# Optimization experiments

Measured on AMD Instinct MI355X. Metric: run time of the kernel, lower is better.

## Reference

```python
import jax, jax.numpy as jnp
import numpy as np

B, S, T, V, E, H = 32, 64, 64, 32000, 256, 512


def lstm_layer(x, h0, c0, Wih, Whh, bih, bhh):
    """PyTorch-convention LSTM layer. x: [B,T,in]; gates order i,f,g,o."""
    xg = jnp.einsum('bti,gi->btg', x, Wih) + (bih + bhh)  # [B,T,4H] precomputed input gates

    def step(carry, xt):
        h, c = carry
        g = xt + h @ Whh.T
        i, f, gg, o = jnp.split(g, 4, axis=-1)
        c = jax.nn.sigmoid(f) * c + jax.nn.sigmoid(i) * jnp.tanh(gg)
        h = jax.nn.sigmoid(o) * jnp.tanh(c)
        return (h, c), h

    (hT, cT), ys = jax.lax.scan(step, (h0, c0), xg.transpose(1, 0, 2))
    return ys.transpose(1, 0, 2), hT, cT


def setup_inputs() -> dict:
    key = jax.random.key(0)
    ks = jax.random.split(key, 32)
    w = lambda k, shape: jax.random.normal(k, shape, jnp.float32) * 0.05
    return {
        'source': jax.random.randint(ks[0], (B, S), 0, V),
        'target': jax.random.randint(ks[1], (B, T), 0, V),
        'enc_emb': w(ks[2], (V, E)),
        'enc_Wih0': w(ks[3], (4 * H, E)),
        'enc_Whh0': w(ks[4], (4 * H, H)),
        'enc_bih0': w(ks[5], (4 * H,)),
        'enc_bhh0': w(ks[6], (4 * H,)),
        'enc_Wih1': w(ks[7], (4 * H, H)),
        'enc_Whh1': w(ks[8], (4 * H, H)),
        'enc_bih1': w(ks[9], (4 * H,)),
        'enc_bhh1': w(ks[10], (4 * H,)),
        'dec_emb': w(ks[11], (V, E)),
        'dec_Wih0': w(ks[12], (4 * H, E)),
        'dec_Whh0': w(ks[13], (4 * H, H)),
        'dec_bih0': w(ks[14], (4 * H,)),
        'dec_bhh0': w(ks[15], (4 * H,)),
        'dec_Wih1': w(ks[16], (4 * H, H)),
        'dec_Whh1': w(ks[17], (4 * H, H)),
        'dec_bih1': w(ks[18], (4 * H,)),
        'dec_bhh1': w(ks[19], (4 * H,)),
        'aff_W': w(ks[20], (V, H)),
        'aff_b': w(ks[21], (V,)),
    }


def reference(source, target, enc_emb, enc_Wih0, enc_Whh0, enc_bih0, enc_bhh0,
              enc_Wih1, enc_Whh1, enc_bih1, enc_bhh1, dec_emb,
              dec_Wih0, dec_Whh0, dec_bih0, dec_bhh0,
              dec_Wih1, dec_Whh1, dec_bih1, dec_bhh1, aff_W, aff_b):
    b = source.shape[0]
    z = jnp.zeros((b, H), jnp.float32)
    # Encoder: 2-layer LSTM over source, keep final (h,c) per layer
    x = enc_emb[source]                                   # [B,S,E]
    y0, h0, c0 = lstm_layer(x, z, z, enc_Wih0, enc_Whh0, enc_bih0, enc_bhh0)
    _, h1, c1 = lstm_layer(y0, z, z, enc_Wih1, enc_Whh1, enc_bih1, enc_bhh1)
    # Decoder: original loop is always teacher-forced (input = target[:, i]),
    # so it equals one full-sequence LSTM over target[:, :-1].
    dx = dec_emb[target[:, :-1]]                          # [B,T-1,E]
    d0, _, _ = lstm_layer(dx, h0, c0, dec_Wih0, dec_Whh0, dec_bih0, dec_bhh0)
    d1, _, _ = lstm_layer(d0, h1, c1, dec_Wih1, dec_Whh1, dec_bih1, dec_bhh1)
    logits = jnp.einsum('bth,vh->btv', d1, aff_W) + aff_b  # [B,T-1,V]
    # outputs[:,0,:] stays zero as in the original
    return jnp.concatenate([jnp.zeros((b, 1, logits.shape[-1]), logits.dtype), logits], axis=1)
```

## Files before the change

kernel.cpp:

```cpp
#include <hip/hip_runtime.h>
#include <hip/hip_bf16.h>

using bf16 = __hip_bfloat16;
typedef __bf16 bf16x8 __attribute__((ext_vector_type(8)));
typedef float f32x4 __attribute__((ext_vector_type(4)));
typedef int i32x4 __attribute__((ext_vector_type(4)));
typedef short short4v __attribute__((ext_vector_type(4)));
typedef short short8v __attribute__((ext_vector_type(8)));

#define DEV __device__ __forceinline__


DEV unsigned short f2bf(float f) {
  unsigned u = __builtin_bit_cast(unsigned, f);
  u = (u + 0x7fffu + ((u >> 16) & 1u)) >> 16;
  return (unsigned short)u;
}

DEV f32x4 mfma16(bf16x8 a, bf16x8 b, f32x4 c) {
  return __builtin_amdgcn_mfma_f32_16x16x32_bf16(a, b, c, 0, 0, 0);
}

DEV void llc_load16(bf16x8* dst, const bf16* p) {
  i32x4 r;
  asm volatile("global_load_dwordx4 %0, %1, off sc0 sc1" : "=v"(r) : "v"(p) : "memory");
  *dst = __builtin_bit_cast(bf16x8, r);
}
DEV void g_load16(bf16x8* dst, const bf16* p) {
  i32x4 r;
  asm volatile("global_load_dwordx4 %0, %1, off" : "=v"(r) : "v"(p) : "memory");
  *dst = __builtin_bit_cast(bf16x8, r);
}
DEV void llc_store16(void* p, short8v v) {
  asm volatile("global_store_dwordx4 %0, %1, off sc0 sc1"
               :: "v"(p), "v"(__builtin_bit_cast(i32x4, v)) : "memory");
}
DEV void llc_store_f32(float* p, float v) {
  asm volatile("global_store_dword %0, %1, off sc0 sc1" :: "v"(p), "v"(v) : "memory");
}
DEV bool valid16(bf16x8 v) {
  i32x4 u = __builtin_bit_cast(i32x4, v);
  return (u[0] != -1) && (u[1] != -1) && (u[2] != -1) && (u[3] != -1);
}

DEV void poll_slab(const bf16* base, int fl, int koff, bf16x8 a0[4], bf16x8 a1[4]) {
  const bf16* r0 = base + (long)fl * 512 + koff;
  const bf16* r1 = base + (long)(fl + 16) * 512 + koff;
#pragma unroll
  for (int kt = 0; kt < 4; ++kt) {
    llc_load16(&a0[kt], r0 + kt * 32);
    llc_load16(&a1[kt], r1 + kt * 32);
  }
  asm volatile("s_waitcnt vmcnt(0)" ::: "memory");
  {
    bool ok = true;
#pragma unroll
    for (int kt = 0; kt < 4; ++kt) ok = ok && valid16(a0[kt]) && valid16(a1[kt]);
    if (__all(ok)) return;
  }
  while (true) {
    unsigned s0, s1, s2, s3;
    asm volatile(
        "global_load_dword %0, %4, off sc0 sc1\n\t"
        "global_load_dword %1, %5, off sc0 sc1\n\t"
        "global_load_dword %2, %6, off sc0 sc1\n\t"
        "global_load_dword %3, %7, off sc0 sc1\n\t"
        "s_waitcnt vmcnt(0)"
        : "=v"(s0), "=v"(s1), "=v"(s2), "=v"(s3)
        : "v"(r0), "v"(r0 + 32), "v"(r0 + 64), "v"(r0 + 96)
        : "memory");
    bool ok = (s0 != 0xFFFFFFFFu) & (s1 != 0xFFFFFFFFu) & (s2 != 0xFFFFFFFFu) &
              (s3 != 0xFFFFFFFFu);
    if (__all(ok)) break;
    __builtin_amdgcn_s_sleep(1);
  }
  while (true) {
#pragma unroll
    for (int kt = 0; kt < 4; ++kt) {
      llc_load16(&a0[kt], r0 + kt * 32);
      llc_load16(&a1[kt], r1 + kt * 32);
    }
    asm volatile("s_waitcnt vmcnt(0)" ::: "memory");
    bool ok = true;
#pragma unroll
    for (int kt = 0; kt < 4; ++kt) ok = ok && valid16(a0[kt]) && valid16(a1[kt]);
    if (__all(ok)) break;
    __builtin_amdgcn_s_sleep(1);
  }
}
DEV float llc_poll_f32(const float* p) {
  while (true) {
    float r;
    asm volatile("global_load_dword %0, %1, off sc0 sc1\n\ts_waitcnt vmcnt(0)"
                 : "=v"(r) : "v"(p) : "memory");
    if (__all(__builtin_bit_cast(unsigned, r) != 0xFFFFFFFFu)) return r;
    __builtin_amdgcn_s_sleep(1);
  }
}

DEV bf16* swz(bf16* base, int row, int colbyte) {
  return (bf16*)((char*)base + row * 128 + (colbyte ^ ((row & 7) << 4)));
}

struct ConvJobs {
  const float* src[9];
  bf16* dst[9];
  int n[9];
  int cnt;
};

__global__ void convert_all(ConvJobs jobs) {
  long base = (long)blockIdx.x * blockDim.x + threadIdx.x;
  long stride = (long)gridDim.x * blockDim.x;
  for (int ji = 0; ji < jobs.cnt; ++ji) {
    const float* s = jobs.src[ji];
    bf16* d = jobs.dst[ji];
    long n4 = (long)jobs.n[ji] >> 2;
    for (long i = base; i < n4; i += stride) {
      f32x4 v = *(const f32x4*)(s + i * 4);
      short4v o;
#pragma unroll
      for (int j = 0; j < 4; ++j) o[j] = (short)f2bf(v[j]);
      *(short4v*)((short*)d + i * 4) = o;
    }
  }
}

__global__ void embed_gather(const int* __restrict__ ids, const float* __restrict__ emb,
                             bf16* __restrict__ out, int rows, int ids_stride) {
  long total = (long)rows * 64;
  long stride = (long)gridDim.x * blockDim.x;
  for (long i = (long)blockIdx.x * blockDim.x + threadIdx.x; i < total; i += stride) {
    int row = (int)(i >> 6);
    int e = ((int)i & 63) * 4;
    int b = row & 31;
    int t = row >> 5;
    int id = ids[b * ids_stride + t];
    f32x4 v = *(const f32x4*)(emb + (long)id * 256 + e);
    short4v o;
#pragma unroll
    for (int j = 0; j < 4; ++j) o[j] = (short)f2bf(v[j]);
    *(short4v*)((short*)out + (long)row * 256 + e) = o;
  }
}

__global__ void zero_t0(float* __restrict__ out) {
  long total = 32l * 8000;
  long stride = (long)gridDim.x * blockDim.x;
  f32x4 z{};
  for (long i = (long)blockIdx.x * blockDim.x + threadIdx.x; i < total; i += stride) {
    long b = i / 8000;
    long v = i - b * 8000;
    *(f32x4*)(out + b * 64 * 32000 + v * 4) = z;
  }
}

__launch_bounds__(256)
__global__ void gemm_aff(const bf16* __restrict__ Ag, const bf16* __restrict__ Wg,
                         const float* __restrict__ affb, float* __restrict__ out) {
  __shared__ __align__(16) bf16 As[128 * 64];
  __shared__ __align__(16) bf16 Bs[128 * 64];
  int mt = blockIdx.x & 15;
  int ns = blockIdx.x >> 4;
  long m0 = (long)mt * 128, gn0 = (long)ns * 128;
  int tid = threadIdx.x;
  int lane = tid & 63, wave = tid >> 6;
  int wm = wave & 1, wn = wave >> 1;
  int fl = lane & 15, fg = lane >> 4;

  if (mt == 0) {
    f32x4 z{};
#pragma unroll
    for (int idx = 0; idx < 4; ++idx) {
      int i = idx * 256 + tid;
      int r = i >> 5, c4 = i & 31;
      *(f32x4*)(out + (long)r * 64 * 32000 + gn0 + c4 * 4) = z;
    }
  }

  f32x4 acc[4][4] = {};
  bf16x8 areg[4], wreg[4];
  int rowv[4], colv[4];
#pragma unroll
  for (int i = 0; i < 4; ++i) {
    int e = (i * 256 + tid) * 8;
    rowv[i] = e >> 6; colv[i] = e & 63;
    long ar = m0 + rowv[i]; if (ar >= 2016) ar = 2015;
    g_load16(&areg[i], Ag + ar * 512 + colv[i]);
    g_load16(&wreg[i], Wg + (gn0 + rowv[i]) * 512 + colv[i]);
  }
  for (int k0 = 0; k0 < 512; k0 += 64) {
    asm volatile("s_waitcnt vmcnt(0)" ::: "memory");
    __syncthreads();
#pragma unroll
    for (int i = 0; i < 4; ++i) {
      *(bf16x8*)swz(As, rowv[i], colv[i] * 2) = areg[i];
      *(bf16x8*)swz(Bs, rowv[i], colv[i] * 2) = wreg[i];
    }
    __syncthreads();
    if (k0 + 64 < 512) {
#pragma unroll
      for (int i = 0; i < 4; ++i) {
        long ar = m0 + rowv[i]; if (ar >= 2016) ar = 2015;
        g_load16(&areg[i], Ag + ar * 512 + (k0 + 64) + colv[i]);
        g_load16(&wreg[i], Wg + (gn0 + rowv[i]) * 512 + (k0 + 64) + colv[i]);
      }
    }
#pragma unroll
    for (int kt = 0; kt < 2; ++kt) {
      bf16x8 af[4], bfr[4];
#pragma unroll
      for (int x = 0; x < 4; ++x)
        af[x] = *(const bf16x8*)swz(As, wm * 64 + x * 16 + fl, (kt * 32 + fg * 8) * 2);
#pragma unroll
      for (int x = 0; x < 4; ++x)
        bfr[x] = *(const bf16x8*)swz(Bs, wn * 64 + x * 16 + fl, (kt * 32 + fg * 8) * 2);
#pragma unroll
      for (int mi = 0; mi < 4; ++mi)
#pragma unroll
        for (int ni = 0; ni < 4; ++ni)
          acc[mi][ni] = mfma16(af[mi], bfr[ni], acc[mi][ni]);
    }
  }
#pragma unroll
  for (int mi = 0; mi < 4; ++mi)
#pragma unroll
    for (int ni = 0; ni < 4; ++ni)
#pragma unroll
      for (int r = 0; r < 4; ++r) {
        long row = m0 + wm * 64 + mi * 16 + fg * 4 + r;
        long col = gn0 + wn * 64 + ni * 16 + fl;
        if (row < 2016) {
          float v = acc[mi][ni][r] + affb[col];
          long orow = (long)(row & 31) * 64 + (row >> 5) + 1;
          out[orow * 32000 + col] = v;
        }
      }
}

__launch_bounds__(256)
__global__ void gemm_fb(const bf16* __restrict__ A, const float* __restrict__ Wf,
                        const float* __restrict__ bias1, float* __restrict__ C,
                        int M, int N, int K) {
  __shared__ __align__(16) bf16 As[128][64];
  __shared__ __align__(16) bf16 Bs[128][64];
  int nm = (M + 127) >> 7;
  int mt_blk = blockIdx.x % nm;
  int nt_blk = blockIdx.x / nm;
  long m0 = (long)mt_blk * 128, n0 = (long)nt_blk * 128;
  int tid = threadIdx.x;
  int lane = tid & 63, wave = tid >> 6;
  int wm = wave & 1, wn = wave >> 1;
  int fl = lane & 15, fg = lane >> 4;
  f32x4 acc[4][4] = {};
  for (int k0 = 0; k0 < K; k0 += 64) {
    __syncthreads();
#pragma unroll
    for (int i = 0; i < 4; ++i) {
      int e = (i * 256 + tid) * 8;
      int row = e >> 6, col = e & 63;
      long ar = m0 + row; if (ar >= M) ar = M - 1;
      *(bf16x8*)(&As[row][col]) = *(const bf16x8*)(A + ar * (long)K + k0 + col);
      long br = n0 + row; if (br >= N) br = N - 1;
      const float* p = Wf + br * (long)K + k0 + col;
      f32x4 v0 = *(const f32x4*)p, v1 = *(const f32x4*)(p + 4);
      short8v o;
#pragma unroll
      for (int j = 0; j < 4; ++j) { o[j] = (short)f2bf(v0[j]); o[j + 4] = (short)f2bf(v1[j]); }
      *(short8v*)(&Bs[row][col]) = o;
    }
    __syncthreads();
#pragma unroll
    for (int kt = 0; kt < 2; ++kt) {
      bf16x8 af[4], bfr[4];
#pragma unroll
      for (int x = 0; x < 4; ++x)
        af[x] = *(const bf16x8*)(&As[wm * 64 + x * 16 + fl][kt * 32 + fg * 8]);
#pragma unroll
      for (int x = 0; x < 4; ++x)
        bfr[x] = *(const bf16x8*)(&Bs[wn * 64 + x * 16 + fl][kt * 32 + fg * 8]);
#pragma unroll
      for (int mi = 0; mi < 4; ++mi)
#pragma unroll
        for (int ni = 0; ni < 4; ++ni)
          acc[mi][ni] = mfma16(af[mi], bfr[ni], acc[mi][ni]);
    }
  }
#pragma unroll
  for (int mi = 0; mi < 4; ++mi)
#pragma unroll
    for (int ni = 0; ni < 4; ++ni)
#pragma unroll
      for (int r = 0; r < 4; ++r) {
        long row = m0 + wm * 64 + mi * 16 + fg * 4 + r;
        long col = n0 + wn * 64 + ni * 16 + fl;
        if (row < M && col < N) {
          float v = acc[mi][ni][r] + bias1[col];
          long orow = (long)(row & 31) * 64 + (row >> 5) + 1;
          C[orow * (long)N + col] = v;
        }
      }
}

struct FusedParams {
  const bf16* wih[4]; const bf16* whh[4];
  const float* bih[4]; const float* bhh[4];
  const bf16* x[4];
  bf16* y[4];
  const bf16* hinit[4];
  const float* cinit[4];
  float* cfin[4];
};

__launch_bounds__(256)
__global__ void lstm_fused(FusedParams P) {
  __shared__ float part[4][32][33];
  __shared__ __align__(16) unsigned short h_sh[32][8];
  const int tid = threadIdx.x;
  const int lane = tid & 63, wave = tid >> 6;
  const int fl = lane & 15, fg = lane >> 4;
  const int l = blockIdx.x >> 6;
  const int slc = blockIdx.x & 63;
  const int n0 = slc * 8;
  const int b_t = tid & 31, d_t = tid >> 5;
  const int T = (l < 2) ? 64 : 63;
  const int Kx = (l & 1) ? 512 : 256;
  const int xspan = Kx >> 2;
  const int ktx = xspan >> 5;
  const bf16* __restrict__ Wih = P.wih[l];
  const bf16* __restrict__ Whh = P.whh[l];
  const bf16* __restrict__ X = P.x[l];
  bf16* __restrict__ Y = P.y[l];
  const bf16* __restrict__ Hinit = P.hinit[l];

  float bsum[4];
#pragma unroll
  for (int gi = 0; gi < 4; ++gi)
    bsum[gi] = P.bih[l][gi * 512 + n0 + d_t] + P.bhh[l][gi * 512 + n0 + d_t];

  bf16x8 wfx[2][4], wfh[2][4];
#pragma unroll
  for (int nt = 0; nt < 2; ++nt) {
    int j = nt * 16 + fl;
    long row = (long)(j >> 3) * 512 + n0 + (j & 7);
#pragma unroll
    for (int kt = 0; kt < 4; ++kt) {
      if (kt < ktx)
        wfx[nt][kt] =
            *(const bf16x8*)(Wih + row * (long)Kx + wave * xspan + kt * 32 + fg * 8);
      wfh[nt][kt] = *(const bf16x8*)(Whh + row * 512l + wave * 128 + kt * 32 + fg * 8);
    }
  }
  float c = 0.f;

  for (int t = 0; t < T; ++t) {
    const bf16* xb = X + (long)t * 32 * Kx;
    f32x4 acc[2][2] = {};
    if (l & 1) {
      bf16x8 xa0[4], xa1[4];
      poll_slab(xb, fl, wave * 128 + fg * 8, xa0, xa1);
#pragma unroll
      for (int kt = 0; kt < 4; ++kt) {
        acc[0][0] = mfma16(xa0[kt], wfx[0][kt], acc[0][0]);
        acc[0][1] = mfma16(xa0[kt], wfx[1][kt], acc[0][1]);
        acc[1][0] = mfma16(xa1[kt], wfx[0][kt], acc[1][0]);
        acc[1][1] = mfma16(xa1[kt], wfx[1][kt], acc[1][1]);
      }
    } else {
      bf16x8 xa0[2], xa1[2];
#pragma unroll
      for (int kt = 0; kt < 2; ++kt) {
        int k = wave * xspan + kt * 32 + fg * 8;
        xa0[kt] = *(const bf16x8*)(xb + (long)fl * Kx + k);
        xa1[kt] = *(const bf16x8*)(xb + (long)(fl + 16) * Kx + k);
      }
#pragma unroll
      for (int kt = 0; kt < 2; ++kt) {
        acc[0][0] = mfma16(xa0[kt], wfx[0][kt], acc[0][0]);
        acc[0][1] = mfma16(xa0[kt], wfx[1][kt], acc[0][1]);
        acc[1][0] = mfma16(xa1[kt], wfx[0][kt], acc[1][0]);
        acc[1][1] = mfma16(xa1[kt], wfx[1][kt], acc[1][1]);
      }
    }

    const bf16* hb = (t == 0) ? Hinit : (Y + (long)(t - 1) * 32 * 512);
    bf16x8 ha0[4], ha1[4];
    poll_slab(hb, fl, wave * 128 + fg * 8, ha0, ha1);
    if (t == 0) c = llc_poll_f32(P.cinit[l] + (long)b_t * 512 + n0 + d_t);
#pragma unroll
    for (int kt = 0; kt < 4; ++kt) {
      acc[0][0] = mfma16(ha0[kt], wfh[0][kt], acc[0][0]);
      acc[0][1] = mfma16(ha0[kt], wfh[1][kt], acc[0][1]);
      acc[1][0] = mfma16(ha1[kt], wfh[0][kt], acc[1][0]);
      acc[1][1] = mfma16(ha1[kt], wfh[1][kt], acc[1][1]);
    }
#pragma unroll
    for (int mt = 0; mt < 2; ++mt)
#pragma unroll
      for (int nt = 0; nt < 2; ++nt)
#pragma unroll
        for (int r = 0; r < 4; ++r)
          part[wave][mt * 16 + fg * 4 + r][nt * 16 + fl] = acc[mt][nt][r];
    __syncthreads();

    float g4[4];
#pragma unroll
    for (int gi = 0; gi < 4; ++gi) {
      int j = gi * 8 + d_t;
      g4[gi] = part[0][b_t][j] + part[1][b_t][j] + part[2][b_t][j] + part[3][b_t][j] +
               bsum[gi];
    }
    float ig = 1.f / (1.f + __expf(-g4[0]));
    float ff = 1.f / (1.f + __expf(-g4[1]));
    float gg = tanhf(g4[2]);
    float og = 1.f / (1.f + __expf(-g4[3]));
    c = ff * c + ig * gg;
    float h = og * tanhf(c);
    h_sh[b_t][d_t] = f2bf(h);
    if (t == T - 1)
      llc_store_f32(P.cfin[l] + (long)b_t * 512 + n0 + d_t, c);
    __syncthreads();
    if (wave == 0 && lane < 32)
      llc_store16((unsigned short*)Y + ((long)t * 32 + lane) * 512 + n0,
                  *(const short8v*)(&h_sh[lane][0]));
  }
}

extern "C" void kernel_launch(void* const* d_in, const int* in_sizes, int n_in,
                              void* d_out, int out_size, void* d_ws, size_t ws_size,
                              hipStream_t stream) {
  (void)in_sizes; (void)n_in; (void)out_size;
  const int*   source   = (const int*)d_in[0];
  const int*   target   = (const int*)d_in[1];
  const float* enc_emb  = (const float*)d_in[2];
  const float* enc_Wih0 = (const float*)d_in[3];
  const float* enc_Whh0 = (const float*)d_in[4];
  const float* enc_bih0 = (const float*)d_in[5];
  const float* enc_bhh0 = (const float*)d_in[6];
  const float* enc_Wih1 = (const float*)d_in[7];
  const float* enc_Whh1 = (const float*)d_in[8];
  const float* enc_bih1 = (const float*)d_in[9];
  const float* enc_bhh1 = (const float*)d_in[10];
  const float* dec_emb  = (const float*)d_in[11];
  const float* dec_Wih0 = (const float*)d_in[12];
  const float* dec_Whh0 = (const float*)d_in[13];
  const float* dec_bih0 = (const float*)d_in[14];
  const float* dec_bhh0 = (const float*)d_in[15];
  const float* dec_Wih1 = (const float*)d_in[16];
  const float* dec_Whh1 = (const float*)d_in[17];
  const float* dec_bih1 = (const float*)d_in[18];
  const float* dec_bhh1 = (const float*)d_in[19];
  const float* aff_W    = (const float*)d_in[20];
  const float* aff_b    = (const float*)d_in[21];
  float* out = (float*)d_out;

  size_t off = 0;
  auto alc = [&](size_t bytes) {
    char* p = (char*)d_ws + off;
    off += (bytes + 255) & ~(size_t)255;
    return (void*)p;
  };
  bf16*  ZH  = (bf16*)alc(32 * 512 * 2);
  float* ZC  = (float*)alc(32 * 512 * 4);
  size_t zero_span = off;
  size_t poison_begin = off;
  float* CE0 = (float*)alc(32 * 512 * 4);
  float* CE1 = (float*)alc(32 * 512 * 4);
  bf16*  YE0 = (bf16*)alc((size_t)2048 * 512 * 2);
  bf16*  YE1 = (bf16*)alc((size_t)2048 * 512 * 2);
  bf16*  YD0 = (bf16*)alc((size_t)2016 * 512 * 2);
  bf16*  YD1 = (bf16*)alc((size_t)2016 * 512 * 2);
  size_t poison_end = off;
  float* CD  = (float*)alc(32 * 512 * 4);
  float* CD2 = (float*)alc(32 * 512 * 4);
  bf16*  XE  = (bf16*)alc((size_t)2048 * 256 * 2);
  bf16*  XD  = (bf16*)alc((size_t)2016 * 256 * 2);
  bf16*  WI0E = (bf16*)alc((size_t)2048 * 256 * 2);
  bf16*  WH0E = (bf16*)alc((size_t)2048 * 512 * 2);
  bf16*  WI1E = (bf16*)alc((size_t)2048 * 512 * 2);
  bf16*  WH1E = (bf16*)alc((size_t)2048 * 512 * 2);
  bf16*  WI0D = (bf16*)alc((size_t)2048 * 256 * 2);
  bf16*  WH0D = (bf16*)alc((size_t)2048 * 512 * 2);
  bf16*  WI1D = (bf16*)alc((size_t)2048 * 512 * 2);
  bf16*  WH1D = (bf16*)alc((size_t)2048 * 512 * 2);
  bf16*  WAFF = (bf16*)alc((size_t)32000 * 512 * 2);
  bool use_waff = (off <= ws_size);

  hipMemsetAsync(d_ws, 0, zero_span, stream);
  hipMemsetAsync((char*)d_ws + poison_begin, 0xFF, poison_end - poison_begin, stream);

  ConvJobs cj;
  cj.src[0] = enc_Wih0; cj.dst[0] = WI0E; cj.n[0] = 2048 * 256;
  cj.src[1] = enc_Whh0; cj.dst[1] = WH0E; cj.n[1] = 2048 * 512;
  cj.src[2] = enc_Wih1; cj.dst[2] = WI1E; cj.n[2] = 2048 * 512;
  cj.src[3] = enc_Whh1; cj.dst[3] = WH1E; cj.n[3] = 2048 * 512;
  cj.src[4] = dec_Wih0; cj.dst[4] = WI0D; cj.n[4] = 2048 * 256;
  cj.src[5] = dec_Whh0; cj.dst[5] = WH0D; cj.n[5] = 2048 * 512;
  cj.src[6] = dec_Wih1; cj.dst[6] = WI1D; cj.n[6] = 2048 * 512;
  cj.src[7] = dec_Whh1; cj.dst[7] = WH1D; cj.n[7] = 2048 * 512;
  cj.cnt = 8;
  if (use_waff) {
    cj.src[8] = aff_W; cj.dst[8] = WAFF; cj.n[8] = 32000 * 512; cj.cnt = 9;
  }
  convert_all<<<dim3(1024), dim3(256), 0, stream>>>(cj);

  embed_gather<<<dim3(512), dim3(256), 0, stream>>>(source, enc_emb, XE, 2048, 64);
  embed_gather<<<dim3(512), dim3(256), 0, stream>>>(target, dec_emb, XD, 2016, 64);
  if (!use_waff) zero_t0<<<dim3(1000), dim3(256), 0, stream>>>(out);

  FusedParams P;
  P.wih[0] = WI0E; P.whh[0] = WH0E; P.bih[0] = enc_bih0; P.bhh[0] = enc_bhh0;
  P.wih[1] = WI1E; P.whh[1] = WH1E; P.bih[1] = enc_bih1; P.bhh[1] = enc_bhh1;
  P.wih[2] = WI0D; P.whh[2] = WH0D; P.bih[2] = dec_bih0; P.bhh[2] = dec_bhh0;
  P.wih[3] = WI1D; P.whh[3] = WH1D; P.bih[3] = dec_bih1; P.bhh[3] = dec_bhh1;
  P.x[0] = XE;  P.x[1] = YE0; P.x[2] = XD;  P.x[3] = YD0;
  P.y[0] = YE0; P.y[1] = YE1; P.y[2] = YD0; P.y[3] = YD1;
  P.hinit[0] = ZH; P.hinit[1] = ZH;
  P.hinit[2] = YE0 + (size_t)63 * 32 * 512;
  P.hinit[3] = YE1 + (size_t)63 * 32 * 512;
  P.cinit[0] = ZC;  P.cinit[1] = ZC;  P.cinit[2] = CE0; P.cinit[3] = CE1;
  P.cfin[0]  = CE0; P.cfin[1]  = CE1; P.cfin[2]  = CD;  P.cfin[3]  = CD2;
  void* args[1] = {&P};
  hipLaunchCooperativeKernel((void*)lstm_fused, dim3(256), dim3(256), args, 0, stream);

  if (use_waff)
    gemm_aff<<<dim3(16 * 250), dim3(256), 0, stream>>>(YD1, WAFF, aff_b, out);
  else
    gemm_fb<<<dim3(16 * 250), dim3(256), 0, stream>>>(YD1, aff_W, aff_b, out,
                                                      2016, 32000, 512);
}
```

Before: 638.0 us.

## Fuse fp32-to-bf16 weight conversion into LSTM and projection kernels, remap GEMM tiles

Removes the separate convert_all pass and its bf16 weight buffers. The LSTM kernel now converts fp32 weights to bf16 while loading them into registers, and the output-projection GEMM converts fp32 W tiles on the fly before writing them to shared memory. The GEMM block index is remapped so groups of 8 N-tiles iterate over all 16 M-tiles, which should improve L2 reuse of the weights; the grid is padded to 4096 with early exits. The GEMM now reads twice the weight bytes and does conversion math 16 times per weight tile, trading that for skipping one full conversion kernel and its write and re-read of a 32 MB buffer.

Result: slower. 704.8 us (+10.5%).

```diff
diff --git a/kernel.cpp b/kernel.cpp
--- a/kernel.cpp
+++ b/kernel.cpp
@@ -19,6 +19,14 @@
 
 DEV f32x4 mfma16(bf16x8 a, bf16x8 b, f32x4 c) {
   return __builtin_amdgcn_mfma_f32_16x16x32_bf16(a, b, c, 0, 0, 0);
+}
+
+DEV bf16x8 cvt8(const float* p) {
+  f32x4 a = *(const f32x4*)p, b = *(const f32x4*)(p + 4);
+  short8v o;
+#pragma unroll
+  for (int j = 0; j < 4; ++j) { o[j] = (short)f2bf(a[j]); o[j + 4] = (short)f2bf(b[j]); }
+  return __builtin_bit_cast(bf16x8, o);
 }
 
 DEV void llc_load16(bf16x8* dst, const bf16* p) {
@@ -102,30 +110,6 @@
   return (bf16*)((char*)base + row * 128 + (colbyte ^ ((row & 7) << 4)));
 }
 
-struct ConvJobs {
-  const float* src[9];
-  bf16* dst[9];
-  int n[9];
-  int cnt;
-};
-
-__global__ void convert_all(ConvJobs jobs) {
-  long base = (long)blockIdx.x * blockDim.x + threadIdx.x;
-  long stride = (long)gridDim.x * blockDim.x;
-  for (int ji = 0; ji < jobs.cnt; ++ji) {
-    const float* s = jobs.src[ji];
-    bf16* d = jobs.dst[ji];
-    long n4 = (long)jobs.n[ji] >> 2;
-    for (long i = base; i < n4; i += stride) {
-      f32x4 v = *(const f32x4*)(s + i * 4);
-      short4v o;
-#pragma unroll
-      for (int j = 0; j < 4; ++j) o[j] = (short)f2bf(v[j]);
-      *(short4v*)((short*)d + i * 4) = o;
-    }
-  }
-}
-
 __global__ void embed_gather(const int* __restrict__ ids, const float* __restrict__ emb,
                              bf16* __restrict__ out, int rows, int ids_stride) {
   long total = (long)rows * 64;
@@ -144,24 +128,15 @@
   }
 }
 
-__global__ void zero_t0(float* __restrict__ out) {
-  long total = 32l * 8000;
-  long stride = (long)gridDim.x * blockDim.x;
-  f32x4 z{};
-  for (long i = (long)blockIdx.x * blockDim.x + threadIdx.x; i < total; i += stride) {
-    long b = i / 8000;
-    long v = i - b * 8000;
-    *(f32x4*)(out + b * 64 * 32000 + v * 4) = z;
-  }
-}
-
 __launch_bounds__(256)
-__global__ void gemm_aff(const bf16* __restrict__ Ag, const bf16* __restrict__ Wg,
+__global__ void gemm_aff(const bf16* __restrict__ Ag, const float* __restrict__ Wf,
                          const float* __restrict__ affb, float* __restrict__ out) {
   __shared__ __align__(16) bf16 As[128 * 64];
   __shared__ __align__(16) bf16 Bs[128 * 64];
-  int mt = blockIdx.x & 15;
-  int ns = blockIdx.x >> 4;
+  int b = blockIdx.x;
+  int ns = (b & 7) + 8 * (b >> 7);
+  int mt = (b >> 3) & 15;
+  if (ns >= 250) return;
   long m0 = (long)mt * 128, gn0 = (long)ns * 128;
   int tid = threadIdx.x;
   int lane = tid & 63, wave = tid >> 6;
@@ -179,7 +154,8 @@
   }
 
   f32x4 acc[4][4] = {};
-  bf16x8 areg[4], wreg[4];
+  bf16x8 areg[4];
+  f32x4 wv0[4], wv1[4];
   int rowv[4], colv[4];
 #pragma unroll
   for (int i = 0; i < 4; ++i) {
@@ -187,7 +163,9 @@
     rowv[i] = e >> 6; colv[i] = e & 63;
     long ar = m0 + rowv[i]; if (ar >= 2016) ar = 2015;
     g_load16(&areg[i], Ag + ar * 512 + colv[i]);
-    g_load16(&wreg[i], Wg + (gn0 + rowv[i]) * 512 + colv[i]);
+    const float* p = Wf + (gn0 + rowv[i]) * 512l + colv[i];
+    wv0[i] = *(const f32x4*)p;
+    wv1[i] = *(const f32x4*)(p + 4);
   }
   for (int k0 = 0; k0 < 512; k0 += 64) {
     asm volatile("s_waitcnt vmcnt(0)" ::: "memory");
@@ -195,7 +173,13 @@
 #pragma unroll
     for (int i = 0; i < 4; ++i) {
       *(bf16x8*)swz(As, rowv[i], colv[i] * 2) = areg[i];
-      *(bf16x8*)swz(Bs, rowv[i], colv[i] * 2) = wreg[i];
+      short8v o;
+#pragma unroll
+      for (int j = 0; j < 4; ++j) {
+        o[j] = (short)f2bf(wv0[i][j]);
+        o[j + 4] = (short)f2bf(wv1[i][j]);
+      }
+      *(short8v*)swz(Bs, rowv[i], colv[i] * 2) = o;
     }
     __syncthreads();
     if (k0 + 64 < 512) {
@@ -203,7 +187,9 @@
       for (int i = 0; i < 4; ++i) {
         long ar = m0 + rowv[i]; if (ar >= 2016) ar = 2015;
         g_load16(&areg[i], Ag + ar * 512 + (k0 + 64) + colv[i]);
-        g_load16(&wreg[i], Wg + (gn0 + rowv[i]) * 512 + (k0 + 64) + colv[i]);
+        const float* p = Wf + (gn0 + rowv[i]) * 512l + (k0 + 64) + colv[i];
+        wv0[i] = *(const f32x4*)p;
+        wv1[i] = *(const f32x4*)(p + 4);
       }
     }
 #pragma unroll
@@ -238,72 +224,8 @@
       }
 }
 
-__launch_bounds__(256)
-__global__ void gemm_fb(const bf16* __restrict__ A, const float* __restrict__ Wf,
-                        const float* __restrict__ bias1, float* __restrict__ C,
-                        int M, int N, int K) {
-  __shared__ __align__(16) bf16 As[128][64];
-  __shared__ __align__(16) bf16 Bs[128][64];
-  int nm = (M + 127) >> 7;
-  int mt_blk = blockIdx.x % nm;
-  int nt_blk = blockIdx.x / nm;
-  long m0 = (long)mt_blk * 128, n0 = (long)nt_blk * 128;
-  int tid = threadIdx.x;
-  int lane = tid & 63, wave = tid >> 6;
-  int wm = wave & 1, wn = wave >> 1;
-  int fl = lane & 15, fg = lane >> 4;
-  f32x4 acc[4][4] = {};
-  for (int k0 = 0; k0 < K; k0 += 64) {
-    __syncthreads();
-#pragma unroll
-    for (int i = 0; i < 4; ++i) {
-      int e = (i * 256 + tid) * 8;
-      int row = e >> 6, col = e & 63;
-      long ar = m0 + row; if (ar >= M) ar = M - 1;
-      *(bf16x8*)(&As[row][col]) = *(const bf16x8*)(A + ar * (long)K + k0 + col);
-      long br = n0 + row; if (br >= N) br = N - 1;
-      const float* p = Wf + br * (long)K + k0 + col;
-      f32x4 v0 = *(const f32x4*)p, v1 = *(const f32x4*)(p + 4);
-      short8v o;
-#pragma unroll
-      for (int j = 0; j < 4; ++j) { o[j] = (short)f2bf(v0[j]); o[j + 4] = (short)f2bf(v1[j]); }
-      *(short8v*)(&Bs[row][col]) = o;
-    }
-    __syncthreads();
-#pragma unroll
-    for (int kt = 0; kt < 2; ++kt) {
-      bf16x8 af[4], bfr[4];
-#pragma unroll
-      for (int x = 0; x < 4; ++x)
-        af[x] = *(const bf16x8*)(&As[wm * 64 + x * 16 + fl][kt * 32 + fg * 8]);
-#pragma unroll
-      for (int x = 0; x < 4; ++x)
-        bfr[x] = *(const bf16x8*)(&Bs[wn * 64 + x * 16 + fl][kt * 32 + fg * 8]);
-#pragma unroll
-      for (int mi = 0; mi < 4; ++mi)
-#pragma unroll
-        for (int ni = 0; ni < 4; ++ni)
-          acc[mi][ni] = mfma16(af[mi], bfr[ni], acc[mi][ni]);
-    }
-  }
-#pragma unroll
-  for (int mi = 0; mi < 4; ++mi)
-#pragma unroll
-    for (int ni = 0; ni < 4; ++ni)
-#pragma unroll
-      for (int r = 0; r < 4; ++r) {
-        long row = m0 + wm * 64 + mi * 16 + fg * 4 + r;
-        long col = n0 + wn * 64 + ni * 16 + fl;
-        if (row < M && col < N) {
-          float v = acc[mi][ni][r] + bias1[col];
-          long orow = (long)(row & 31) * 64 + (row >> 5) + 1;
-          C[orow * (long)N + col] = v;
-        }
-      }
-}
-
 struct FusedParams {
-  const bf16* wih[4]; const bf16* whh[4];
+  const float* wih[4]; const float* whh[4];
   const float* bih[4]; const float* bhh[4];
   const bf16* x[4];
   bf16* y[4];
@@ -327,8 +249,8 @@
   const int Kx = (l & 1) ? 512 : 256;
   const int xspan = Kx >> 2;
   const int ktx = xspan >> 5;
-  const bf16* __restrict__ Wih = P.wih[l];
-  const bf16* __restrict__ Whh = P.whh[l];
+  const float* __restrict__ WihF = P.wih[l];
+  const float* __restrict__ WhhF = P.whh[l];
   const bf16* __restrict__ X = P.x[l];
   bf16* __restrict__ Y = P.y[l];
   const bf16* __restrict__ Hinit = P.hinit[l];
@@ -346,9 +268,8 @@
 #pragma unroll
     for (int kt = 0; kt < 4; ++kt) {
       if (kt < ktx)
-        wfx[nt][kt] =
-            *(const bf16x8*)(Wih + row * (long)Kx + wave * xspan + kt * 32 + fg * 8);
-      wfh[nt][kt] = *(const bf16x8*)(Whh + row * 512l + wave * 128 + kt * 32 + fg * 8);
+        wfx[nt][kt] = cvt8(WihF + row * (long)Kx + wave * xspan + kt * 32 + fg * 8);
+      wfh[nt][kt] = cvt8(WhhF + row * 512l + wave * 128 + kt * 32 + fg * 8);
     }
   }
   float c = 0.f;
@@ -429,7 +350,7 @@
 extern "C" void kernel_launch(void* const* d_in, const int* in_sizes, int n_in,
                               void* d_out, int out_size, void* d_ws, size_t ws_size,
                               hipStream_t stream) {
-  (void)in_sizes; (void)n_in; (void)out_size;
+  (void)in_sizes; (void)n_in; (void)out_size; (void)ws_size;
   const int*   source   = (const int*)d_in[0];
   const int*   target   = (const int*)d_in[1];
   const float* enc_emb  = (const float*)d_in[2];
@@ -475,44 +396,18 @@
   float* CD2 = (float*)alc(32 * 512 * 4);
   bf16*  XE  = (bf16*)alc((size_t)2048 * 256 * 2);
   bf16*  XD  = (bf16*)alc((size_t)2016 * 256 * 2);
-  bf16*  WI0E = (bf16*)alc((size_t)2048 * 256 * 2);
-  bf16*  WH0E = (bf16*)alc((size_t)2048 * 512 * 2);
-  bf16*  WI1E = (bf16*)alc((size_t)2048 * 512 * 2);
-  bf16*  WH1E = (bf16*)alc((size_t)2048 * 512 * 2);
-  bf16*  WI0D = (bf16*)alc((size_t)2048 * 256 * 2);
-  bf16*  WH0D = (bf16*)alc((size_t)2048 * 512 * 2);
-  bf16*  WI1D = (bf16*)alc((size_t)2048 * 512 * 2);
-  bf16*  WH1D = (bf16*)alc((size_t)2048 * 512 * 2);
-  bf16*  WAFF = (bf16*)alc((size_t)32000 * 512 * 2);
-  bool use_waff = (off <= ws_size);
 
   hipMemsetAsync(d_ws, 0, zero_span, stream);
   hipMemsetAsync((char*)d_ws + poison_begin, 0xFF, poison_end - poison_begin, stream);
 
-  ConvJobs cj;
-  cj.src[0] = enc_Wih0; cj.dst[0] = WI0E; cj.n[0] = 2048 * 256;
-  cj.src[1] = enc_Whh0; cj.dst[1] = WH0E; cj.n[1] = 2048 * 512;
-  cj.src[2] = enc_Wih1; cj.dst[2] = WI1E; cj.n[2] = 2048 * 512;
-  cj.src[3] = enc_Whh1; cj.dst[3] = WH1E; cj.n[3] = 2048 * 512;
-  cj.src[4] = dec_Wih0; cj.dst[4] = WI0D; cj.n[4] = 2048 * 256;
-  cj.src[5] = dec_Whh0; cj.dst[5] = WH0D; cj.n[5] = 2048 * 512;
-  cj.src[6] = dec_Wih1; cj.dst[6] = WI1D; cj.n[6] = 2048 * 512;
-  cj.src[7] = dec_Whh1; cj.dst[7] = WH1D; cj.n[7] = 2048 * 512;
-  cj.cnt = 8;
-  if (use_waff) {
-    cj.src[8] = aff_W; cj.dst[8] = WAFF; cj.n[8] = 32000 * 512; cj.cnt = 9;
-  }
-  convert_all<<<dim3(1024), dim3(256), 0, stream>>>(cj);
-
   embed_gather<<<dim3(512), dim3(256), 0, stream>>>(source, enc_emb, XE, 2048, 64);
   embed_gather<<<dim3(512), dim3(256), 0, stream>>>(target, dec_emb, XD, 2016, 64);
-  if (!use_waff) zero_t0<<<dim3(1000), dim3(256), 0, stream>>>(out);
 
   FusedParams P;
-  P.wih[0] = WI0E; P.whh[0] = WH0E; P.bih[0] = enc_bih0; P.bhh[0] = enc_bhh0;
-  P.wih[1] = WI1E; P.whh[1] = WH1E; P.bih[1] = enc_bih1; P.bhh[1] = enc_bhh1;
-  P.wih[2] = WI0D; P.whh[2] = WH0D; P.bih[2] = dec_bih0; P.bhh[2] = dec_bhh0;
-  P.wih[3] = WI1D; P.whh[3] = WH1D; P.bih[3] = dec_bih1; P.bhh[3] = dec_bhh1;
+  P.wih[0] = enc_Wih0; P.whh[0] = enc_Whh0; P.bih[0] = enc_bih0; P.bhh[0] = enc_bhh0;
+  P.wih[1] = enc_Wih1; P.whh[1] = enc_Whh1; P.bih[1] = enc_bih1; P.bhh[1] = enc_bhh1;
+  P.wih[2] = dec_Wih0; P.whh[2] = dec_Whh0; P.bih[2] = dec_bih0; P.bhh[2] = dec_bhh0;
+  P.wih[3] = dec_Wih1; P.whh[3] = dec_Whh1; P.bih[3] = dec_bih1; P.bhh[3] = dec_bhh1;
   P.x[0] = XE;  P.x[1] = YE0; P.x[2] = XD;  P.x[3] = YD0;
   P.y[0] = YE0; P.y[1] = YE1; P.y[2] = YD0; P.y[3] = YD1;
   P.hinit[0] = ZH; P.hinit[1] = ZH;
@@ -523,9 +418,5 @@
   void* args[1] = {&P};
   hipLaunchCooperativeKernel((void*)lstm_fused, dim3(256), dim3(256), args, 0, stream);
 
-  if (use_waff)
-    gemm_aff<<<dim3(16 * 250), dim3(256), 0, stream>>>(YD1, WAFF, aff_b, out);
-  else
-    gemm_fb<<<dim3(16 * 250), dim3(256), 0, stream>>>(YD1, aff_W, aff_b, out,
-                                                      2016, 32000, 512);
-}
+  gemm_aff<<<dim3(4096), dim3(256), 0, stream>>>(YD1, aff_W, aff_b, out);
+}
```
